# Performance work log

Hardware: AMD Instinct MI355X
Metric: run time of the kernel (lower is better)

## Reference

```python
import jax, jax.numpy as jnp
import numpy as np

OUT, IN = 11008, 4096
B, S = 8, 32


def setup_inputs() -> dict:
    key = jax.random.key(0)
    k_x, k_w, k_s, k_b = jax.random.split(key, 4)
    x = jax.random.normal(k_x, (B, S, IN), dtype=jnp.float32).astype(jnp.float16)
    # int8 weight storage (symmetric quant range [-128, 127])
    w_int8 = jax.random.randint(k_w, (OUT, IN), -128, 128, dtype=jnp.int32).astype(jnp.int8)
    # per-output-channel scale, small positive values typical of int8 quant
    scale = jax.random.uniform(k_s, (OUT,), dtype=jnp.float32) * 0.01 + 1e-4
    bias = (jax.random.normal(k_b, (OUT,), dtype=jnp.float32) * 0.02).astype(jnp.float16)
    return {"x": x, "w_int8": w_int8, "scale": scale, "bias": bias}


def reference(x, w_int8, scale, bias):
    # w_fp[o, i] = int8_weight[o, i] * scale[o]   (on-the-fly dequant)
    w = w_int8.astype(jnp.float32) * scale[:, None]          # [OUT, IN] fp32
    # F.linear: out = x @ w.T + bias, computed in fp32
    out = jnp.einsum('bsi,oi->bso', x.astype(jnp.float32), w) + bias.astype(jnp.float32)
    return out.astype(x.dtype)                                # cast back to x.dtype (fp16)
```

## Files before the change

kernel.cpp:

```cpp
#include <hip/hip_runtime.h>
#include <hip/hip_bf16.h>
#include <stdint.h>

typedef __attribute__((ext_vector_type(8))) __bf16 bf16x8;
typedef __attribute__((ext_vector_type(4))) float f32x4;

constexpr int K_DIM = 4096;
constexpr int N_DIM = 11008;
constexpr int M_DIM = 256;
constexpr int TM = 256;
constexpr int TN = 128;
constexpr int BK = 64;
constexpr int NT = 256;
constexpr int KT_ALL = K_DIM / BK;
constexpr int KSPLIT = 6;

__device__ __forceinline__ void gload_lds16(const __bf16* gptr, __bf16* lptr) {
  __builtin_amdgcn_global_load_lds(
      (const __attribute__((address_space(1))) uint32_t*)gptr,
      (__attribute__((address_space(3))) uint32_t*)lptr, 16, 0, 0);
}

__device__ __forceinline__ bf16x8 cvt8(const float4 u0, const float4 u1) {
  bf16x8 v;
  v[0] = (__bf16)u0.x; v[1] = (__bf16)u0.y; v[2] = (__bf16)u0.z; v[3] = (__bf16)u0.w;
  v[4] = (__bf16)u1.x; v[5] = (__bf16)u1.y; v[6] = (__bf16)u1.z; v[7] = (__bf16)u1.w;
  return v;
}

__global__ void cvt_x_kernel(const float* __restrict__ x, __bf16* __restrict__ ws) {
  const int i = (blockIdx.x * 256 + threadIdx.x) * 8;
  const float4 u0 = ((const float4*)(x + i))[0];
  const float4 u1 = ((const float4*)(x + i))[1];
  *(bf16x8*)(ws + i) = cvt8(u0, u1);
}

template<bool USE_WS>
__global__ __launch_bounds__(NT, 2) void int8_linear_kernel(
    const float* __restrict__ x,
    const __bf16* __restrict__ xws,
    const int*   __restrict__ w,
    const float* __restrict__ scale,
    const float* __restrict__ bias,
    float*       __restrict__ out)
{
  __shared__ __bf16 As[TM * BK];
  __shared__ __bf16 Wsh[2][TN * BK];

  const int tid  = threadIdx.x;
  const int lane = tid & 63;
  const int wv   = tid >> 6;
  const int quad = lane >> 4;
  const int l16  = lane & 15;
  const int wm   = wv >> 1;
  const int wn   = wv & 1;
  const int n_base = blockIdx.x * TN;
  const int kc     = blockIdx.y;

  const int t0 = (kc * KT_ALL) / KSPLIT;
  const int t1 = ((kc + 1) * KT_ALL) / KSPLIT;
  const int ntile = t1 - t0;
  const int k0 = t0 * BK;

  const int wrow = tid >> 1;
  const int wc0  = (tid & 1) * 4;
  const int* wptr = w + (int64_t)(n_base + wrow) * K_DIM + k0 + wc0 * 8;

  f32x4 acc[8][4];
#pragma unroll
  for (int i = 0; i < 8; ++i)
#pragma unroll
    for (int j = 0; j < 4; ++j) acc[i][j] = (f32x4){0.f, 0.f, 0.f, 0.f};

  int4 wr[8];
  auto wload = [&](int t) {
    const int4* p = (const int4*)(wptr + t * BK);
#pragma unroll
    for (int j = 0; j < 8; ++j) wr[j] = p[j];
  };
  auto commitW = [&](__bf16* wbuf) {
#pragma unroll
    for (int j = 0; j < 4; ++j) {
      const int4 a = wr[j * 2], b = wr[j * 2 + 1];
      bf16x8 v;
      v[0] = (__bf16)(float)a.x; v[1] = (__bf16)(float)a.y;
      v[2] = (__bf16)(float)a.z; v[3] = (__bf16)(float)a.w;
      v[4] = (__bf16)(float)b.x; v[5] = (__bf16)(float)b.y;
      v[6] = (__bf16)(float)b.z; v[7] = (__bf16)(float)b.w;
      const int slot = (wc0 + j) ^ (wrow & 7);
      *(bf16x8*)(wbuf + wrow * BK + slot * 8) = v;
    }
  };
  auto a_stage = [&](int t) {
    if (USE_WS) {
#pragma unroll
      for (int j = 0; j < 8; ++j) {
        const int c = j * 256 + tid;
        const int row = c >> 3;
        const int k8 = (c & 7) ^ (row & 7);
        gload_lds16(xws + (int64_t)row * K_DIM + (t0 + t) * BK + k8 * 8, As + c * 8);
      }
    } else {
#pragma unroll
      for (int j = 0; j < 8; ++j) {
        const int c = j * 256 + tid;
        const int row = c >> 3;
        const int k8 = c & 7;
        const float* s = x + (int64_t)row * K_DIM + (t0 + t) * BK + k8 * 8;
        const bf16x8 v = cvt8(((const float4*)s)[0], ((const float4*)s)[1]);
        const int slot = k8 ^ (row & 7);
        *(bf16x8*)(As + row * BK + slot * 8) = v;
      }
    }
  };
  auto compute = [&](const __bf16* wbuf) {
#pragma unroll
    for (int ks = 0; ks < 2; ++ks) {
      bf16x8 a[8], b[4];
#pragma unroll
      for (int mi = 0; mi < 8; ++mi) {
        const int m = wm * 128 + mi * 16 + l16;
        const int slot = (ks * 4 + quad) ^ (m & 7);
        a[mi] = *(const bf16x8*)(As + m * BK + slot * 8);
      }
#pragma unroll
      for (int ni = 0; ni < 4; ++ni) {
        const int n = wn * 64 + ni * 16 + l16;
        const int slot = (ks * 4 + quad) ^ (n & 7);
        b[ni] = *(const bf16x8*)(wbuf + n * BK + slot * 8);
      }
#pragma unroll
      for (int mi = 0; mi < 8; ++mi)
#pragma unroll
        for (int ni = 0; ni < 4; ++ni)
          acc[mi][ni] = __builtin_amdgcn_mfma_f32_16x16x32_bf16(
              a[mi], b[ni], acc[mi][ni], 0, 0, 0);
    }
  };

  wload(0);
  commitW(Wsh[0]);
  a_stage(0);
  __syncthreads();

  for (int t = 0; t < ntile; ++t) {
    const bool more = (t + 1 < ntile);
    if (more) wload(t + 1);
    compute(Wsh[t & 1]);
    if (more) {
      commitW(Wsh[(t + 1) & 1]);
      __syncthreads();
      a_stage(t + 1);
      __syncthreads();
    }
  }

#pragma unroll
  for (int ni = 0; ni < 4; ++ni) {
    const int col = n_base + wn * 64 + ni * 16 + l16;
    const float sc = scale[col];
    const float bi = (kc == 0) ? bias[col] : 0.0f;
#pragma unroll
    for (int mi = 0; mi < 8; ++mi) {
      const int row0 = wm * 128 + mi * 16 + quad * 4;
#pragma unroll
      for (int r = 0; r < 4; ++r)
        unsafeAtomicAdd(out + (int64_t)(row0 + r) * N_DIM + col,
                        acc[mi][ni][r] * sc + bi);
    }
  }
}

extern "C" void kernel_launch(void* const* d_in, const int* in_sizes, int n_in,
                              void* d_out, int out_size, void* d_ws, size_t ws_size,
                              hipStream_t stream) {
  const float* x     = (const float*)d_in[0];
  const int*   w     = (const int*)d_in[1];
  const float* scale = (const float*)d_in[2];
  const float* bias  = (const float*)d_in[3];
  float* out = (float*)d_out;

  __bf16* xws = (__bf16*)d_ws;
  const bool use_ws = ws_size >= (size_t)M_DIM * K_DIM * sizeof(__bf16);

  hipMemsetAsync(out, 0, (size_t)M_DIM * N_DIM * sizeof(float), stream);

  dim3 grid(N_DIM / TN, KSPLIT), block(NT);
  if (use_ws) {
    cvt_x_kernel<<<M_DIM * K_DIM / (256 * 8), 256, 0, stream>>>(x, xws);
    int8_linear_kernel<true><<<grid, block, 0, stream>>>(x, xws, w, scale, bias, out);
  } else {
    int8_linear_kernel<false><<<grid, block, 0, stream>>>(x, xws, w, scale, bias, out);
  }
}
```

Baseline: 326.8 us.

## Double-buffer A and W tiles with single barrier per k-step and smaller N tile

Shrinks the N tile to 64 and doubles threads to 512 (8 waves covering 256x64), halving split-K. A and W LDS tiles are double-buffered, and the loop is unrolled by two with explicit vmcnt/lgkmcnt waits and one barrier per tile instead of two. The goal is to overlap the global->LDS staging of the next tile with MFMA compute and cut barrier stalls. Smaller per-wave tiles lower register pressure, but each wave now does less compute per LDS read of A, and each block re-reads all of A for half as many columns.

```diff
diff --git a/kernel.cpp b/kernel.cpp
--- a/kernel.cpp
+++ b/kernel.cpp
@@ -9,11 +9,11 @@
 constexpr int N_DIM = 11008;
 constexpr int M_DIM = 256;
 constexpr int TM = 256;
-constexpr int TN = 128;
+constexpr int TN = 64;
 constexpr int BK = 64;
-constexpr int NT = 256;
+constexpr int NT = 512;
 constexpr int KT_ALL = K_DIM / BK;
-constexpr int KSPLIT = 6;
+constexpr int KSPLIT = 3;
 
 __device__ __forceinline__ void gload_lds16(const __bf16* gptr, __bf16* lptr) {
   __builtin_amdgcn_global_load_lds(
@@ -36,7 +36,7 @@
 }
 
 template<bool USE_WS>
-__global__ __launch_bounds__(NT, 2) void int8_linear_kernel(
+__global__ __launch_bounds__(NT, 4) void int8_linear_kernel(
     const float* __restrict__ x,
     const __bf16* __restrict__ xws,
     const int*   __restrict__ w,
@@ -44,7 +44,7 @@
     const float* __restrict__ bias,
     float*       __restrict__ out)
 {
-  __shared__ __bf16 As[TM * BK];
+  __shared__ __bf16 As[2][TM * BK];
   __shared__ __bf16 Wsh[2][TN * BK];
 
   const int tid  = threadIdx.x;
@@ -54,6 +54,7 @@
   const int l16  = lane & 15;
   const int wm   = wv >> 1;
   const int wn   = wv & 1;
+  const int m_base = wm * 64;
   const int n_base = blockIdx.x * TN;
   const int kc     = blockIdx.y;
 
@@ -62,107 +63,134 @@
   const int ntile = t1 - t0;
   const int k0 = t0 * BK;
 
-  const int wrow = tid >> 1;
-  const int wc0  = (tid & 1) * 4;
-  const int* wptr = w + (int64_t)(n_base + wrow) * K_DIM + k0 + wc0 * 8;
-
-  f32x4 acc[8][4];
-#pragma unroll
-  for (int i = 0; i < 8; ++i)
-#pragma unroll
-    for (int j = 0; j < 4; ++j) acc[i][j] = (f32x4){0.f, 0.f, 0.f, 0.f};
-
-  int4 wr[8];
-  auto wload = [&](int t) {
+  const int wrow   = tid >> 3;
+  const int wchunk = tid & 7;
+  const int wslot  = wchunk ^ (wrow & 7);
+  const int* wptr = w + (int64_t)(n_base + wrow) * K_DIM + k0 + wchunk * 8;
+
+  f32x4 acc[4][2];
+#pragma unroll
+  for (int i = 0; i < 4; ++i)
+#pragma unroll
+    for (int j = 0; j < 2; ++j) acc[i][j] = (f32x4){0.f, 0.f, 0.f, 0.f};
+
+  int4 wrA[2], wrB[2];
+  auto wload = [&](int t, int4* wr) {
     const int4* p = (const int4*)(wptr + t * BK);
-#pragma unroll
-    for (int j = 0; j < 8; ++j) wr[j] = p[j];
-  };
-  auto commitW = [&](__bf16* wbuf) {
-#pragma unroll
-    for (int j = 0; j < 4; ++j) {
-      const int4 a = wr[j * 2], b = wr[j * 2 + 1];
-      bf16x8 v;
-      v[0] = (__bf16)(float)a.x; v[1] = (__bf16)(float)a.y;
-      v[2] = (__bf16)(float)a.z; v[3] = (__bf16)(float)a.w;
-      v[4] = (__bf16)(float)b.x; v[5] = (__bf16)(float)b.y;
-      v[6] = (__bf16)(float)b.z; v[7] = (__bf16)(float)b.w;
-      const int slot = (wc0 + j) ^ (wrow & 7);
-      *(bf16x8*)(wbuf + wrow * BK + slot * 8) = v;
-    }
-  };
-  auto a_stage = [&](int t) {
+    wr[0] = p[0]; wr[1] = p[1];
+  };
+  auto commitW = [&](const int4* wr, __bf16* wbuf) {
+    bf16x8 v;
+    v[0] = (__bf16)(float)wr[0].x; v[1] = (__bf16)(float)wr[0].y;
+    v[2] = (__bf16)(float)wr[0].z; v[3] = (__bf16)(float)wr[0].w;
+    v[4] = (__bf16)(float)wr[1].x; v[5] = (__bf16)(float)wr[1].y;
+    v[6] = (__bf16)(float)wr[1].z; v[7] = (__bf16)(float)wr[1].w;
+    *(bf16x8*)(wbuf + wrow * BK + wslot * 8) = v;
+  };
+  auto a_stage = [&](int t, __bf16* abuf) {
     if (USE_WS) {
 #pragma unroll
-      for (int j = 0; j < 8; ++j) {
-        const int c = j * 256 + tid;
+      for (int j = 0; j < 4; ++j) {
+        const int c = j * 512 + tid;
         const int row = c >> 3;
         const int k8 = (c & 7) ^ (row & 7);
-        gload_lds16(xws + (int64_t)row * K_DIM + (t0 + t) * BK + k8 * 8, As + c * 8);
+        gload_lds16(xws + (int64_t)row * K_DIM + (t0 + t) * BK + k8 * 8, abuf + c * 8);
       }
     } else {
 #pragma unroll
-      for (int j = 0; j < 8; ++j) {
-        const int c = j * 256 + tid;
+      for (int j = 0; j < 4; ++j) {
+        const int c = j * 512 + tid;
         const int row = c >> 3;
         const int k8 = c & 7;
         const float* s = x + (int64_t)row * K_DIM + (t0 + t) * BK + k8 * 8;
         const bf16x8 v = cvt8(((const float4*)s)[0], ((const float4*)s)[1]);
         const int slot = k8 ^ (row & 7);
-        *(bf16x8*)(As + row * BK + slot * 8) = v;
-      }
-    }
-  };
-  auto compute = [&](const __bf16* wbuf) {
+        *(bf16x8*)(abuf + row * BK + slot * 8) = v;
+      }
+    }
+  };
+  auto compute = [&](const __bf16* abuf, const __bf16* wbuf) {
 #pragma unroll
     for (int ks = 0; ks < 2; ++ks) {
-      bf16x8 a[8], b[4];
-#pragma unroll
-      for (int mi = 0; mi < 8; ++mi) {
-        const int m = wm * 128 + mi * 16 + l16;
+      bf16x8 a[4], b[2];
+#pragma unroll
+      for (int mi = 0; mi < 4; ++mi) {
+        const int m = m_base + mi * 16 + l16;
         const int slot = (ks * 4 + quad) ^ (m & 7);
-        a[mi] = *(const bf16x8*)(As + m * BK + slot * 8);
-      }
-#pragma unroll
-      for (int ni = 0; ni < 4; ++ni) {
-        const int n = wn * 64 + ni * 16 + l16;
+        a[mi] = *(const bf16x8*)(abuf + m * BK + slot * 8);
+      }
+#pragma unroll
+      for (int ni = 0; ni < 2; ++ni) {
+        const int n = wn * 32 + ni * 16 + l16;
         const int slot = (ks * 4 + quad) ^ (n & 7);
         b[ni] = *(const bf16x8*)(wbuf + n * BK + slot * 8);
       }
 #pragma unroll
-      for (int mi = 0; mi < 8; ++mi)
-#pragma unroll
-        for (int ni = 0; ni < 4; ++ni)
+      for (int mi = 0; mi < 4; ++mi)
+#pragma unroll
+        for (int ni = 0; ni < 2; ++ni)
           acc[mi][ni] = __builtin_amdgcn_mfma_f32_16x16x32_bf16(
               a[mi], b[ni], acc[mi][ni], 0, 0, 0);
     }
   };
 
-  wload(0);
-  commitW(Wsh[0]);
-  a_stage(0);
-  __syncthreads();
-
-  for (int t = 0; t < ntile; ++t) {
-    const bool more = (t + 1 < ntile);
-    if (more) wload(t + 1);
-    compute(Wsh[t & 1]);
-    if (more) {
-      commitW(Wsh[(t + 1) & 1]);
-      __syncthreads();
-      a_stage(t + 1);
-      __syncthreads();
+  wload(0, wrA);
+  __builtin_amdgcn_sched_barrier(0);
+  a_stage(0, As[0]);
+  __builtin_amdgcn_sched_barrier(0);
+  wload(1, wrB);
+  commitW(wrA, Wsh[0]);
+  asm volatile("s_waitcnt vmcnt(2)" ::: "memory");
+  asm volatile("s_waitcnt lgkmcnt(0)" ::: "memory");
+  __builtin_amdgcn_sched_barrier(0);
+  __builtin_amdgcn_s_barrier();
+  __builtin_amdgcn_sched_barrier(0);
+
+  for (int t = 0; t < ntile; t += 2) {
+    {
+      const bool hA = (t + 1 < ntile);
+      const bool hW = (t + 2 < ntile);
+      if (hA) a_stage(t + 1, As[1]);
+      __builtin_amdgcn_sched_barrier(0);
+      if (hW) wload(t + 2, wrA);
+      if (hA) commitW(wrB, Wsh[1]);
+      compute(As[0], Wsh[0]);
+      if (hA) {
+        if (hW) asm volatile("s_waitcnt vmcnt(2)" ::: "memory");
+        else    asm volatile("s_waitcnt vmcnt(0)" ::: "memory");
+        asm volatile("s_waitcnt lgkmcnt(0)" ::: "memory");
+        __builtin_amdgcn_sched_barrier(0);
+        __builtin_amdgcn_s_barrier();
+        __builtin_amdgcn_sched_barrier(0);
+      }
+    }
+    if (t + 1 < ntile) {
+      const bool hA = (t + 2 < ntile);
+      const bool hW = (t + 3 < ntile);
+      if (hA) a_stage(t + 2, As[0]);
+      __builtin_amdgcn_sched_barrier(0);
+      if (hW) wload(t + 3, wrB);
+      if (hA) commitW(wrA, Wsh[0]);
+      compute(As[1], Wsh[1]);
+      if (hA) {
+        if (hW) asm volatile("s_waitcnt vmcnt(2)" ::: "memory");
+        else    asm volatile("s_waitcnt vmcnt(0)" ::: "memory");
+        asm volatile("s_waitcnt lgkmcnt(0)" ::: "memory");
+        __builtin_amdgcn_sched_barrier(0);
+        __builtin_amdgcn_s_barrier();
+        __builtin_amdgcn_sched_barrier(0);
+      }
     }
   }
 
 #pragma unroll
-  for (int ni = 0; ni < 4; ++ni) {
-    const int col = n_base + wn * 64 + ni * 16 + l16;
+  for (int ni = 0; ni < 2; ++ni) {
+    const int col = n_base + wn * 32 + ni * 16 + l16;
     const float sc = scale[col];
     const float bi = (kc == 0) ? bias[col] : 0.0f;
 #pragma unroll
-    for (int mi = 0; mi < 8; ++mi) {
-      const int row0 = wm * 128 + mi * 16 + quad * 4;
+    for (int mi = 0; mi < 4; ++mi) {
+      const int row0 = m_base + mi * 16 + quad * 4;
 #pragma unroll
       for (int r = 0; r < 4; ++r)
         unsafeAtomicAdd(out + (int64_t)(row0 + r) * N_DIM + col,
```

Measured after the change: 306.4 us. 1.07x faster.
